# Kernel optimization log

Hardware: AMD Instinct MI355X
Metric: run time of the kernel (lower is better)

## Reference

```python
import jax, jax.numpy as jnp
import numpy as np

EPS = 1e-8


def setup_inputs() -> dict:
    key = jax.random.key(0)
    k1, k2 = jax.random.split(key)
    N, D, K = 200000, 256, 64
    embeds = jax.random.normal(k1, (N, D), dtype=jnp.float32)
    init = jax.random.uniform(k2, (K, D), dtype=jnp.float32)  # torch.rand(K, n_h)
    beta = jnp.ones((1,), dtype=jnp.float32)
    return {"embeds": embeds, "init": init, "beta": beta, "num_iter": 11}


def reference(embeds, init, beta, num_iter):
    # embeds: [N, D], init: [K, D], beta: scalar temperature
    data_abs = jnp.linalg.norm(embeds, axis=1, keepdims=True)            # [N, 1]
    data_norm = embeds / jnp.maximum(data_abs, EPS)                      # [N, D]
    b = beta.reshape(())
    mu = init
    r = None
    for _ in range(num_iter):  # small fixed iteration count (default 11)
        mu_abs = jnp.linalg.norm(mu, axis=1, keepdims=True)              # [K, 1]
        mu_norm = mu / jnp.maximum(mu_abs, EPS)                          # [K, D]
        dist = data_norm @ mu_norm.T                                     # [N, K]
        r = jax.nn.softmax(b * dist, axis=1)                             # [N, K]
        cluster_r = r.sum(axis=0)                                        # [K]
        cluster_mean = r.T @ embeds                                      # [K, D]
        mu = cluster_mean / cluster_r[:, None]                           # diag(1/cluster_r) @ cluster_mean
    return mu, r
```

## Files before the change

kernel.cpp:

```cpp
#include <hip/hip_runtime.h>
#include <math.h>


#define N_ROWS 200000
#define DIM 256
#define KC 64
#define NUM_ITER 11
#define TR 64
#define NTILES (N_ROWS / TR)
#define EPSV 1e-8f
#define NB 256

typedef _Float16 half8 __attribute__((ext_vector_type(8)));
typedef _Float16 half4 __attribute__((ext_vector_type(4)));
typedef float f32x4 __attribute__((ext_vector_type(4)));

typedef __attribute__((address_space(3))) void as3_void;
typedef __attribute__((address_space(1))) void as1_void;

__device__ __forceinline__ void glds16(const void* g, void* l) {
  __builtin_amdgcn_global_load_lds((const as1_void*)g, (as3_void*)l, 16, 0, 0);
}

__device__ __forceinline__ float wave_reduce_sum(float v) {
#pragma unroll
  for (int off = 32; off > 0; off >>= 1) v += __shfl_xor(v, off, 64);
  return v;
}

__device__ __forceinline__ void barrier_lgkm_only() {
  __builtin_amdgcn_sched_barrier(0);
  asm volatile("s_waitcnt lgkmcnt(0)" ::: "memory");
  __builtin_amdgcn_s_barrier();
  __builtin_amdgcn_sched_barrier(0);
}

__global__ void rn_convert_kernel(const float* __restrict__ embeds,
                                  float* __restrict__ inv_norm,
                                  _Float16* __restrict__ Xh,
                                  const float* __restrict__ init,
                                  float* __restrict__ mu_raw,
                                  float* __restrict__ mu_ssq) {
  if (blockIdx.x == 0) {
    const int c = threadIdx.x >> 2, qq = threadIdx.x & 3;
    const float4* src = (const float4*)(init + (size_t)c * DIM + 64 * qq);
    float4* dst = (float4*)(mu_raw + (size_t)c * DIM + 64 * qq);
    float ss = 0.f;
#pragma unroll
    for (int i = 0; i < 16; ++i) {
      float4 v = src[i];
      dst[i] = v;
      ss = fmaf(v.x, v.x, ss); ss = fmaf(v.y, v.y, ss);
      ss = fmaf(v.z, v.z, ss); ss = fmaf(v.w, v.w, ss);
    }
    mu_ssq[c * 4 + qq] = ss;
  }
  int gw = (blockIdx.x * blockDim.x + threadIdx.x) >> 6;
  int lane = threadIdx.x & 63;
  int nw = (gridDim.x * blockDim.x) >> 6;
  for (int row = gw; row < N_ROWS; row += nw) {
    float4 v = *(const float4*)(embeds + (size_t)row * DIM + 4 * lane);
    float s = v.x * v.x;
    s = fmaf(v.y, v.y, s); s = fmaf(v.z, v.z, s); s = fmaf(v.w, v.w, s);
    s = wave_reduce_sum(s);
    if (lane == 0) inv_norm[row] = 1.0f / fmaxf(sqrtf(s), EPSV);
    half4 h;
    h[0] = (_Float16)v.x; h[1] = (_Float16)v.y; h[2] = (_Float16)v.z; h[3] = (_Float16)v.w;
    *(half4*)(Xh + (size_t)row * DIM + 4 * lane) = h;
  }
}

__device__ __forceinline__ void stage_row512_8(const _Float16* g, _Float16* l,
                                               int wid, int lane) {
#pragma unroll
  for (int ii = 0; ii < 4; ++ii) {
    int i = wid * 4 + ii;
    int row = i * 2 + (lane >> 5);
    int slot = (lane & 31) ^ (row & 7);
    glds16((const char*)g + row * 512 + slot * 16, (char*)l + i * 1024);
  }
}

template <int LAST>
__global__ __launch_bounds__(512, 2) void cluster_main8(
    const _Float16* __restrict__ Xh, const float* __restrict__ inv_norm,
    const float* __restrict__ beta, const float* __restrict__ mu_raw,
    const float* __restrict__ mu_ssq, float* __restrict__ part_cm,
    float* __restrict__ part_crt, float* __restrict__ r_out) {
  __shared__ alignas(16) _Float16 mu_lds[KC * DIM];
  __shared__ alignas(16) _Float16 x_lds[3][TR * DIM];
  __shared__ alignas(16) _Float16 r_lds[KC * TR];
  __shared__ float cr_lds[4 * KC];

  const int tid = threadIdx.x, wid = tid >> 6, lane = tid & 63;
  const int l15 = lane & 15, h = lane >> 4;
  const float b = beta[0];
  const int myrow = 16 * (wid & 3) + l15;
  const int rb0 = blockIdx.x;

  stage_row512_8(Xh + (size_t)rb0 * TR * DIM, x_lds[0], wid, lane);
  stage_row512_8(Xh + (size_t)(rb0 + NB) * TR * DIM, x_lds[1], wid, lane);

  if (tid < KC) {
    const float4 s4 = *(const float4*)&mu_ssq[4 * tid];
    cr_lds[tid] = 1.0f / fmaxf(sqrtf(s4.x + s4.y + s4.z + s4.w), EPSV);
  }
  barrier_lgkm_only();
  {
    const float4* mu_raw4 = (const float4*)mu_raw;
#pragma unroll
    for (int i = 0; i < 8; ++i) {
      const int idx = tid + 512 * i;
      const int cl = idx >> 6;
      const int dim0 = (idx & 63) * 4;
      float4 v = mu_raw4[idx];
      const float iv = cr_lds[cl];
      const int sw = dim0 ^ ((cl & 7) << 3);
      half4 hh;
      hh[0] = (_Float16)(v.x * iv); hh[1] = (_Float16)(v.y * iv);
      hh[2] = (_Float16)(v.z * iv); hh[3] = (_Float16)(v.w * iv);
      *(half4*)&mu_lds[cl * DIM + sw] = hh;
    }
  }
  asm volatile("s_waitcnt vmcnt(4)" ::: "memory");
  barrier_lgkm_only();

  f32x4 acc2[4][2] = {};
  float cr_acc[16] = {};
  int idx3 = 0;
  for (int rb = rb0; rb < NTILES; rb += NB) {
    _Float16* xb = x_lds[idx3];
    const int i2 = (idx3 + 2 >= 3) ? idx3 - 1 : idx3 + 2;
    const bool have1 = (rb + NB < NTILES), have2 = (rb + 2 * NB < NTILES);
    if (!LAST && have2)
      stage_row512_8(Xh + (size_t)(rb + 2 * NB) * TR * DIM, x_lds[i2], wid, lane);

    f32x4 acc1[4] = {};
    uint4 tin[8];
    if (wid < 4) {
#pragma unroll
      for (int t = 0; t < 8; ++t) {
        const int kb = 32 * t + 8 * h;
        half8 bx = *(const half8*)&xb[myrow * DIM + (kb ^ ((myrow & 7) << 3))];
#pragma unroll
        for (int m = 0; m < 4; ++m) {
          const int cl = 16 * m + l15;
          half8 am = *(const half8*)&mu_lds[cl * DIM + (kb ^ ((cl & 7) << 3))];
          acc1[m] = __builtin_amdgcn_mfma_f32_16x16x32_f16(am, bx, acc1[m], 0, 0, 0);
        }
      }
    } else {
      const int t8 = tid & 255;
      const int db = t8 >> 3, rb8 = t8 & 7;
#pragma unroll
      for (int k2 = 0; k2 < 8; ++k2)
        tin[k2] = *(const uint4*)&xb[(8 * rb8 + k2) * DIM + ((8 * db) ^ (k2 << 3))];
    }
    barrier_lgkm_only();

    if (wid < 4) {
      const int xr = rb * TR + myrow;
      const float sc = b * inv_norm[xr];
#pragma unroll
      for (int m = 0; m < 4; ++m)
#pragma unroll
        for (int j = 0; j < 4; ++j) acc1[m][j] *= sc;
      float mx = -1e30f;
#pragma unroll
      for (int m = 0; m < 4; ++m)
#pragma unroll
        for (int j = 0; j < 4; ++j) mx = fmaxf(mx, acc1[m][j]);
      mx = fmaxf(mx, __shfl_xor(mx, 16));
      mx = fmaxf(mx, __shfl_xor(mx, 32));
      float esum = 0.f;
#pragma unroll
      for (int m = 0; m < 4; ++m)
#pragma unroll
        for (int j = 0; j < 4; ++j) {
          float e = __expf(acc1[m][j] - mx);
          acc1[m][j] = e;
          esum += e;
        }
      esum += __shfl_xor(esum, 16);
      esum += __shfl_xor(esum, 32);
      const float rcp = 1.0f / esum;
#pragma unroll
      for (int m = 0; m < 4; ++m) {
#pragma unroll
        for (int j = 0; j < 4; ++j) {
          const float rv = acc1[m][j] * rcp;
          acc1[m][j] = rv;
          const int cl = 16 * m + 4 * h + j;
          cr_acc[m * 4 + j] += rv;
          r_lds[cl * TR + (myrow ^ ((cl & 7) << 3))] = (_Float16)rv;
        }
        if (LAST)
          *(float4*)&r_out[(size_t)xr * KC + 16 * m + 4 * h] = *(float4*)&acc1[m];
      }
    } else {
      const int t8 = tid & 255;
      const int db = t8 >> 3, rb8 = t8 & 7;
      union U { uint4 v; unsigned u[4]; };
#pragma unroll
      for (int j = 0; j < 8; ++j) {
        const unsigned sel = (j & 1) ? 0x07060302u : 0x05040100u;
        U o;
#pragma unroll
        for (int m2 = 0; m2 < 4; ++m2)
          o.u[m2] = __builtin_amdgcn_perm(((const unsigned*)&tin[2 * m2 + 1])[j >> 1],
                                          ((const unsigned*)&tin[2 * m2])[j >> 1], sel);
        *(uint4*)&xb[(8 * db + j) * TR + 8 * (rb8 ^ j)] = o.v;
      }
    }
    if (LAST && have2)
      stage_row512_8(Xh + (size_t)(rb + 2 * NB) * TR * DIM, x_lds[i2], wid, lane);
    barrier_lgkm_only();

#pragma unroll
    for (int t = 0; t < 2; ++t) {
      const int kb = 32 * t + 8 * h;
      half8 ar[4], bx2[2];
#pragma unroll
      for (int m = 0; m < 4; ++m) {
        const int cl = 16 * m + l15;
        ar[m] = *(const half8*)&r_lds[cl * TR + (kb ^ ((cl & 7) << 3))];
      }
#pragma unroll
      for (int n = 0; n < 2; ++n) {
        const int dm = 32 * wid + 16 * n + l15;
        bx2[n] = *(const half8*)&xb[dm * TR + (kb ^ ((dm & 7) << 3))];
      }
#pragma unroll
      for (int m = 0; m < 4; ++m)
#pragma unroll
        for (int n = 0; n < 2; ++n)
          acc2[m][n] = __builtin_amdgcn_mfma_f32_16x16x32_f16(ar[m], bx2[n], acc2[m][n], 0, 0, 0);
    }

    if (have1) {
      if (have2) asm volatile("s_waitcnt vmcnt(4)" ::: "memory");
      else       asm volatile("s_waitcnt vmcnt(0)" ::: "memory");
      barrier_lgkm_only();
    }
    idx3 = (idx3 + 1 == 3) ? 0 : idx3 + 1;
  }

  float* pc = part_cm + (size_t)blockIdx.x * (KC * DIM);
#pragma unroll
  for (int m = 0; m < 4; ++m)
#pragma unroll
    for (int n = 0; n < 2; ++n)
#pragma unroll
      for (int j = 0; j < 4; ++j)
        pc[(16 * m + 4 * h + j) * DIM + 32 * wid + 16 * n + l15] = acc2[m][n][j];
  if (wid < 4) {
#pragma unroll
    for (int m = 0; m < 4; ++m)
#pragma unroll
      for (int j = 0; j < 4; ++j) {
        float v = cr_acc[m * 4 + j];
        v += __shfl_xor(v, 1); v += __shfl_xor(v, 2);
        v += __shfl_xor(v, 4); v += __shfl_xor(v, 8);
        if (l15 == 0) cr_lds[wid * KC + 16 * m + 4 * h + j] = v;
      }
  }
  __syncthreads();
  if (wid == 0)
    part_crt[(size_t)lane * NB + blockIdx.x] =
        cr_lds[lane] + cr_lds[KC + lane] + cr_lds[2 * KC + lane] + cr_lds[3 * KC + lane];
}

template <int FINAL>
__global__ void reduce_mu(const float* __restrict__ part_cm,
                          const float* __restrict__ part_crt,
                          float* __restrict__ mu_raw, float* __restrict__ mu_ssq,
                          float* __restrict__ mu_out) {
  const int cl = blockIdx.x, q = blockIdx.y;
  const int tid = threadIdx.x, wid = tid >> 6, lane = tid & 63;
  __shared__ float red2[4 * 64];
  __shared__ float cr4[4];
  float c = part_crt[(size_t)cl * NB + tid];
  c = wave_reduce_sum(c);
  if (lane == 0) cr4[wid] = c;
  float s = 0.f;
  const float* basep =
      part_cm + (size_t)(64 * wid) * (KC * DIM) + cl * DIM + 64 * q + lane;
#pragma unroll 8
  for (int i = 0; i < 64; ++i) s += basep[(size_t)i * (KC * DIM)];
  red2[wid * 64 + lane] = s;
  __syncthreads();
  if (wid == 0) {
    const float crv = cr4[0] + cr4[1] + cr4[2] + cr4[3];
    const float st = red2[lane] + red2[64 + lane] + red2[128 + lane] + red2[192 + lane];
    const float mu = st / crv;
    const int dim = 64 * q + lane;
    if (FINAL) {
      mu_out[cl * DIM + dim] = mu;
    } else {
      mu_raw[cl * DIM + dim] = mu;
      float ss = wave_reduce_sum(mu * mu);
      if (lane == 0) mu_ssq[cl * 4 + q] = ss;
    }
  }
}

__global__ void rownorm_v1(const float* __restrict__ embeds, float* __restrict__ inv_norm) {
  int gw = (blockIdx.x * blockDim.x + threadIdx.x) >> 6;
  int lane = threadIdx.x & 63;
  int nw = (gridDim.x * blockDim.x) >> 6;
  for (int row = gw; row < N_ROWS; row += nw) {
    const float* rp = embeds + (size_t)row * DIM;
    float s = 0.f;
#pragma unroll
    for (int j = 0; j < 4; ++j) { float v = rp[lane + 64 * j]; s = fmaf(v, v, s); }
    s = wave_reduce_sum(s);
    if (lane == 0) inv_norm[row] = 1.0f / fmaxf(sqrtf(s), EPSV);
  }
}
__global__ void prep0_v1(const float* __restrict__ init, float* __restrict__ muT) {
  int k = blockIdx.x, lane = threadIdx.x;
  const float* rp = init + k * DIM;
  float v[4]; float s = 0.f;
#pragma unroll
  for (int j = 0; j < 4; ++j) { v[j] = rp[lane + 64 * j]; s = fmaf(v[j], v[j], s); }
  s = wave_reduce_sum(s);
  float inv = 1.0f / fmaxf(sqrtf(s), EPSV);
#pragma unroll
  for (int j = 0; j < 4; ++j) muT[(lane + 64 * j) * KC + k] = v[j] * inv;
}
__device__ __forceinline__ float wave_reduce_max_v1(float v) {
#pragma unroll
  for (int off = 32; off > 0; off >>= 1) v = fmaxf(v, __shfl_xor(v, off, 64));
  return v;
}
template <int LAST>
__global__ __launch_bounds__(256, 1) void main_v1(
    const float* __restrict__ embeds, const float* __restrict__ inv_norm,
    const float* __restrict__ muT, const float* __restrict__ beta,
    float* __restrict__ part_cm, float* __restrict__ part_cr,
    float* __restrict__ r_out, int nb) {
  __shared__ float mu_l[DIM * KC];
  __shared__ float x_l[TR * DIM];
  __shared__ float r_l[TR * KC];
  __shared__ float cr_l[4 * KC];
  const int tid = threadIdx.x, wid = tid >> 6, lane = tid & 63;
  const float b = beta[0];
  {
    const float4* m4 = (const float4*)muT; float4* ml4 = (float4*)mu_l;
#pragma unroll
    for (int i = 0; i < 16; ++i) ml4[tid + i * 256] = m4[tid + i * 256];
  }
  float acc[64];
#pragma unroll
  for (int i = 0; i < 64; ++i) acc[i] = 0.f;
  float cr = 0.f;
  for (int rb = blockIdx.x; rb < NTILES; rb += nb) {
    const int row0 = rb * TR;
    __syncthreads();
    {
      const float4* x4 = (const float4*)(embeds + (size_t)row0 * DIM);
      float4* xl4 = (float4*)x_l;
#pragma unroll
      for (int i = 0; i < 16; ++i) xl4[tid + i * 256] = x4[tid + i * 256];
    }
    __syncthreads();
    float dist[16];
#pragma unroll
    for (int r = 0; r < 16; ++r) dist[r] = 0.f;
    const int rbase = wid * 16;
    for (int d = 0; d < DIM; d += 4) {
      float mv0 = mu_l[(d + 0) * KC + lane], mv1 = mu_l[(d + 1) * KC + lane];
      float mv2 = mu_l[(d + 2) * KC + lane], mv3 = mu_l[(d + 3) * KC + lane];
#pragma unroll
      for (int r = 0; r < 16; ++r) {
        float4 xv = *(const float4*)&x_l[(rbase + r) * DIM + d];
        dist[r] = fmaf(xv.x, mv0, dist[r]); dist[r] = fmaf(xv.y, mv1, dist[r]);
        dist[r] = fmaf(xv.z, mv2, dist[r]); dist[r] = fmaf(xv.w, mv3, dist[r]);
      }
    }
#pragma unroll
    for (int r = 0; r < 16; ++r) {
      const int row = rbase + r;
      float s = b * (dist[r] * inv_norm[row0 + row]);
      float m = wave_reduce_max_v1(s);
      float e = __expf(s - m);
      float sum = wave_reduce_sum(e);
      float rv = e * (1.0f / sum);
      cr += rv;
      r_l[row * KC + lane] = rv;
      if (LAST) r_out[(size_t)(row0 + row) * KC + lane] = rv;
    }
    __syncthreads();
    const int dbase = wid * 64;
    for (int row = 0; row < TR; ++row) {
      float rv = r_l[row * KC + lane];
#pragma unroll
      for (int dd = 0; dd < 64; dd += 4) {
        float4 xv = *(const float4*)&x_l[row * DIM + dbase + dd];
        acc[dd + 0] = fmaf(rv, xv.x, acc[dd + 0]); acc[dd + 1] = fmaf(rv, xv.y, acc[dd + 1]);
        acc[dd + 2] = fmaf(rv, xv.z, acc[dd + 2]); acc[dd + 3] = fmaf(rv, xv.w, acc[dd + 3]);
      }
    }
  }
  {
    float* pp = part_cm + ((size_t)blockIdx.x * KC + lane) * DIM + wid * 64;
#pragma unroll
    for (int dd = 0; dd < 64; dd += 4)
      *(float4*)&pp[dd] = make_float4(acc[dd], acc[dd + 1], acc[dd + 2], acc[dd + 3]);
    cr_l[wid * KC + lane] = cr;
  }
  __syncthreads();
  if (wid == 0) {
    float c = cr_l[lane] + cr_l[64 + lane] + cr_l[128 + lane] + cr_l[192 + lane];
    part_cr[(size_t)blockIdx.x * KC + lane] = c;
  }
}
template <int FINAL>
__global__ void reduce_v1(const float* __restrict__ part_cm, const float* __restrict__ part_cr,
                          float* __restrict__ muT, float* __restrict__ mu_out, int nb) {
  const int k = blockIdx.x, t = threadIdx.x;
  __shared__ float red[256];
  float s = 0.f;
  for (int bl = 0; bl < nb; ++bl) s += part_cm[((size_t)bl * KC + k) * DIM + t];
  float c = 0.f;
  for (int bl = t; bl < nb; bl += 256) c += part_cr[(size_t)bl * KC + k];
  red[t] = c; __syncthreads();
#pragma unroll
  for (int off = 128; off > 0; off >>= 1) { if (t < off) red[t] += red[t + off]; __syncthreads(); }
  const float crv = red[0]; __syncthreads();
  const float mu = s / crv;
  if (FINAL) { mu_out[k * DIM + t] = mu; return; }
  red[t] = mu * mu; __syncthreads();
#pragma unroll
  for (int off = 128; off > 0; off >>= 1) { if (t < off) red[t] += red[t + off]; __syncthreads(); }
  const float inv = 1.0f / fmaxf(sqrtf(red[0]), EPSV);
  muT[t * KC + k] = mu * inv;
}

extern "C" void kernel_launch(void* const* d_in, const int* in_sizes, int n_in,
                              void* d_out, int out_size, void* d_ws, size_t ws_size,
                              hipStream_t stream) {
  const float* embeds = (const float*)d_in[0];
  const float* init = (const float*)d_in[1];
  const float* beta = (const float*)d_in[2];
  float* out_mu = (float*)d_out;
  float* out_r = out_mu + KC * DIM;
  char* ws = (char*)d_ws;

  const size_t szX = (size_t)N_ROWS * DIM * 2;
  const size_t szInv = (size_t)N_ROWS * 4;
  const size_t szMuR = (size_t)KC * DIM * 4;
  const size_t szSsq = (size_t)KC * 4 * 4;
  const size_t szPC = (size_t)NB * KC * DIM * 4;
  const size_t szPR = (size_t)KC * NB * 4;
  const size_t need = szX + szInv + szMuR + szSsq + szPC + szPR;

  if (ws_size >= need) {
    char* pp = ws;
    _Float16* Xh = (_Float16*)pp; pp += szX;
    float* invn = (float*)pp; pp += szInv;
    float* mu_raw = (float*)pp; pp += szMuR;
    float* mu_ssq = (float*)pp; pp += szSsq;
    float* pcm = (float*)pp; pp += szPC;
    float* pcrt = (float*)pp;

    rn_convert_kernel<<<2048, 256, 0, stream>>>(embeds, invn, Xh, init, mu_raw, mu_ssq);
    for (int it = 0; it < NUM_ITER; ++it) {
      if (it > 0)
        reduce_mu<0><<<dim3(KC, 4), 256, 0, stream>>>(pcm, pcrt, mu_raw, mu_ssq, nullptr);
      if (it == NUM_ITER - 1)
        cluster_main8<1><<<NB, 512, 0, stream>>>(Xh, invn, beta, mu_raw, mu_ssq,
                                                 pcm, pcrt, out_r);
      else
        cluster_main8<0><<<NB, 512, 0, stream>>>(Xh, invn, beta, mu_raw, mu_ssq,
                                                 pcm, pcrt, out_r);
    }
    reduce_mu<1><<<dim3(KC, 4), 256, 0, stream>>>(pcm, pcrt, nullptr, nullptr, out_mu);
  } else {
    float* wsf = (float*)d_ws;
    float* muT = wsf;
    float* invn = muT + DIM * KC;
    size_t avail = ws_size / sizeof(float);
    size_t fixed = (size_t)DIM * KC + N_ROWS;
    size_t per_blk = (size_t)KC * DIM + KC;
    int nb = 256;
    if (avail > fixed) {
      size_t mx = (avail - fixed) / per_blk;
      if (mx < 256) nb = (int)mx;
    } else nb = 1;
    if (nb < 1) nb = 1;
    float* pcm = invn + N_ROWS;
    float* pcr = pcm + (size_t)nb * KC * DIM;

    rownorm_v1<<<2048, 256, 0, stream>>>(embeds, invn);
    prep0_v1<<<KC, 64, 0, stream>>>(init, muT);
    for (int it = 0; it < NUM_ITER; ++it) {
      if (it > 0) reduce_v1<0><<<KC, 256, 0, stream>>>(pcm, pcr, muT, nullptr, nb);
      if (it == NUM_ITER - 1)
        main_v1<1><<<nb, 256, 0, stream>>>(embeds, invn, muT, beta, pcm, pcr, out_r, nb);
      else
        main_v1<0><<<nb, 256, 0, stream>>>(embeds, invn, muT, beta, pcm, pcr, nullptr, nb);
    }
    reduce_v1<1><<<KC, 256, 0, stream>>>(pcm, pcr, muT, out_mu, nb);
  }
}
```

Measured before the change: 581.3 us.

## Split distance GEMM across all eight waves with register-resident centroids

The distance MFMA, previously done by four waves while the other four only loaded the transpose data, is now split over the K dimension across all eight waves. Partial sums pass through a new LDS buffer and are combined before the softmax. Normalized centroid fragments are held in registers instead of being re-read from LDS every tile. The per-block inverse norms are prefetched into LDS, and the transpose writes into a separate xt buffer. This adds an extra LDS round trip for the partial sums, more register pressure, and modified vmcnt wait accounting.

```diff
diff --git a/kernel.cpp b/kernel.cpp
--- a/kernel.cpp
+++ b/kernel.cpp
@@ -87,39 +87,59 @@
     const float* __restrict__ beta, const float* __restrict__ mu_raw,
     const float* __restrict__ mu_ssq, float* __restrict__ part_cm,
     float* __restrict__ part_crt, float* __restrict__ r_out) {
-  __shared__ alignas(16) _Float16 mu_lds[KC * DIM];
   __shared__ alignas(16) _Float16 x_lds[3][TR * DIM];
+  __shared__ alignas(16) _Float16 xt_lds[DIM * TR];
   __shared__ alignas(16) _Float16 r_lds[KC * TR];
+  __shared__ alignas(16) f32x4 dist_lds[16 * 64];
   __shared__ float cr_lds[4 * KC];
+  __shared__ float inv_lds[16 * 64];
 
   const int tid = threadIdx.x, wid = tid >> 6, lane = tid & 63;
   const int l15 = lane & 15, h = lane >> 4;
+  const int kh = wid >> 2, rg = wid & 3;
   const float b = beta[0];
-  const int myrow = 16 * (wid & 3) + l15;
+  const int myrow = 16 * rg + l15;
   const int rb0 = blockIdx.x;
-
+  const int ntb = (NTILES - 1 - rb0) / NB + 1;
+
+  float4 s4;
+  if (tid < KC) s4 = *(const float4*)&mu_ssq[4 * tid];
+  float4 mv[8];
+  {
+    const float4* mu_raw4 = (const float4*)mu_raw;
+#pragma unroll
+    for (int i = 0; i < 8; ++i) mv[i] = mu_raw4[tid + 512 * i];
+  }
+  if (wid < 4) {
+    int ig = 4 * wid + (lane >> 4);
+    if (ig > ntb - 1) ig = ntb - 1;
+    glds16((const char*)inv_norm + (size_t)(rb0 + ig * NB) * (TR * 4) + (lane & 15) * 16,
+           (char*)inv_lds + wid * 1024);
+  }
   stage_row512_8(Xh + (size_t)rb0 * TR * DIM, x_lds[0], wid, lane);
   stage_row512_8(Xh + (size_t)(rb0 + NB) * TR * DIM, x_lds[1], wid, lane);
-
-  if (tid < KC) {
-    const float4 s4 = *(const float4*)&mu_ssq[4 * tid];
-    cr_lds[tid] = 1.0f / fmaxf(sqrtf(s4.x + s4.y + s4.z + s4.w), EPSV);
-  }
+  if (tid < KC) cr_lds[tid] = 1.0f / fmaxf(sqrtf(s4.x + s4.y + s4.z + s4.w), EPSV);
   barrier_lgkm_only();
-  {
-    const float4* mu_raw4 = (const float4*)mu_raw;
-#pragma unroll
-    for (int i = 0; i < 8; ++i) {
-      const int idx = tid + 512 * i;
-      const int cl = idx >> 6;
-      const int dim0 = (idx & 63) * 4;
-      float4 v = mu_raw4[idx];
-      const float iv = cr_lds[cl];
-      const int sw = dim0 ^ ((cl & 7) << 3);
-      half4 hh;
-      hh[0] = (_Float16)(v.x * iv); hh[1] = (_Float16)(v.y * iv);
-      hh[2] = (_Float16)(v.z * iv); hh[3] = (_Float16)(v.w * iv);
-      *(half4*)&mu_lds[cl * DIM + sw] = hh;
+#pragma unroll
+  for (int i = 0; i < 8; ++i) {
+    const int idx = tid + 512 * i;
+    const int cl = idx >> 6;
+    const int dim0 = (idx & 63) * 4;
+    const float iv = cr_lds[cl];
+    half4 hh;
+    hh[0] = (_Float16)(mv[i].x * iv); hh[1] = (_Float16)(mv[i].y * iv);
+    hh[2] = (_Float16)(mv[i].z * iv); hh[3] = (_Float16)(mv[i].w * iv);
+    *(half4*)&xt_lds[cl * DIM + (dim0 ^ ((cl & 7) << 3))] = hh;
+  }
+  barrier_lgkm_only();
+  half8 amreg[4][4];
+#pragma unroll
+  for (int t = 0; t < 4; ++t) {
+    const int kb = 128 * kh + 32 * t + 8 * h;
+#pragma unroll
+    for (int m = 0; m < 4; ++m) {
+      const int cl = 16 * m + l15;
+      amreg[t][m] = *(const half8*)&xt_lds[cl * DIM + (kb ^ ((cl & 7) << 3))];
     }
   }
   asm volatile("s_waitcnt vmcnt(4)" ::: "memory");
@@ -128,7 +148,8 @@
   f32x4 acc2[4][2] = {};
   float cr_acc[16] = {};
   int idx3 = 0;
-  for (int rb = rb0; rb < NTILES; rb += NB) {
+  int ti = 0;
+  for (int rb = rb0; rb < NTILES; rb += NB, ++ti) {
     _Float16* xb = x_lds[idx3];
     const int i2 = (idx3 + 2 >= 3) ? idx3 - 1 : idx3 + 2;
     const bool have1 = (rb + NB < NTILES), have2 = (rb + 2 * NB < NTILES);
@@ -136,31 +157,25 @@
       stage_row512_8(Xh + (size_t)(rb + 2 * NB) * TR * DIM, x_lds[i2], wid, lane);
 
     f32x4 acc1[4] = {};
-    uint4 tin[8];
-    if (wid < 4) {
-#pragma unroll
-      for (int t = 0; t < 8; ++t) {
-        const int kb = 32 * t + 8 * h;
-        half8 bx = *(const half8*)&xb[myrow * DIM + (kb ^ ((myrow & 7) << 3))];
-#pragma unroll
-        for (int m = 0; m < 4; ++m) {
-          const int cl = 16 * m + l15;
-          half8 am = *(const half8*)&mu_lds[cl * DIM + (kb ^ ((cl & 7) << 3))];
-          acc1[m] = __builtin_amdgcn_mfma_f32_16x16x32_f16(am, bx, acc1[m], 0, 0, 0);
-        }
-      }
-    } else {
-      const int t8 = tid & 255;
-      const int db = t8 >> 3, rb8 = t8 & 7;
-#pragma unroll
-      for (int k2 = 0; k2 < 8; ++k2)
-        tin[k2] = *(const uint4*)&xb[(8 * rb8 + k2) * DIM + ((8 * db) ^ (k2 << 3))];
+#pragma unroll
+    for (int t = 0; t < 4; ++t) {
+      const int kb = 128 * kh + 32 * t + 8 * h;
+      half8 bx = *(const half8*)&xb[myrow * DIM + (kb ^ ((myrow & 7) << 3))];
+#pragma unroll
+      for (int m = 0; m < 4; ++m)
+        acc1[m] = __builtin_amdgcn_mfma_f32_16x16x32_f16(amreg[t][m], bx, acc1[m], 0, 0, 0);
+    }
+    if (kh) {
+#pragma unroll
+      for (int m = 0; m < 4; ++m) dist_lds[(rg * 4 + m) * 64 + lane] = acc1[m];
     }
     barrier_lgkm_only();
 
-    if (wid < 4) {
+    if (!kh) {
+#pragma unroll
+      for (int m = 0; m < 4; ++m) acc1[m] += dist_lds[(rg * 4 + m) * 64 + lane];
       const int xr = rb * TR + myrow;
-      const float sc = b * inv_norm[xr];
+      const float sc = b * inv_lds[ti * 64 + myrow];
 #pragma unroll
       for (int m = 0; m < 4; ++m)
 #pragma unroll
@@ -201,15 +216,19 @@
       const int t8 = tid & 255;
       const int db = t8 >> 3, rb8 = t8 & 7;
       union U { uint4 v; unsigned u[4]; };
+      U tin[8];
+#pragma unroll
+      for (int k2 = 0; k2 < 8; ++k2)
+        tin[k2].v = *(const uint4*)&xb[(8 * rb8 + k2) * DIM + ((8 * db) ^ (k2 << 3))];
 #pragma unroll
       for (int j = 0; j < 8; ++j) {
         const unsigned sel = (j & 1) ? 0x07060302u : 0x05040100u;
         U o;
 #pragma unroll
         for (int m2 = 0; m2 < 4; ++m2)
-          o.u[m2] = __builtin_amdgcn_perm(((const unsigned*)&tin[2 * m2 + 1])[j >> 1],
-                                          ((const unsigned*)&tin[2 * m2])[j >> 1], sel);
-        *(uint4*)&xb[(8 * db + j) * TR + 8 * (rb8 ^ j)] = o.v;
+          o.u[m2] = __builtin_amdgcn_perm(tin[2 * m2 + 1].u[j >> 1],
+                                          tin[2 * m2].u[j >> 1], sel);
+        *(uint4*)&xt_lds[(8 * db + j) * TR + 8 * (rb8 ^ j)] = o.v;
       }
     }
     if (LAST && have2)
@@ -228,7 +247,7 @@
 #pragma unroll
       for (int n = 0; n < 2; ++n) {
         const int dm = 32 * wid + 16 * n + l15;
-        bx2[n] = *(const half8*)&xb[dm * TR + (kb ^ ((dm & 7) << 3))];
+        bx2[n] = *(const half8*)&xt_lds[dm * TR + (kb ^ ((dm & 7) << 3))];
       }
 #pragma unroll
       for (int m = 0; m < 4; ++m)
@@ -238,8 +257,15 @@
     }
 
     if (have1) {
-      if (have2) asm volatile("s_waitcnt vmcnt(4)" ::: "memory");
-      else       asm volatile("s_waitcnt vmcnt(0)" ::: "memory");
+      if (!have2) {
+        asm volatile("s_waitcnt vmcnt(0)" ::: "memory");
+      } else if (!LAST) {
+        asm volatile("s_waitcnt vmcnt(4)" ::: "memory");
+      } else if (!kh) {
+        asm volatile("s_waitcnt vmcnt(8)" ::: "memory");
+      } else {
+        asm volatile("s_waitcnt vmcnt(4)" ::: "memory");
+      }
       barrier_lgkm_only();
     }
     idx3 = (idx3 + 1 == 3) ? 0 : idx3 + 1;
```

After: 536.9 us. 7.6% less time.
